# Performance work log

Hardware: AMD Instinct MI355X
Metric: run time of the kernel (lower is better)

## Reference

```python
import jax, jax.numpy as jnp
import numpy as np

NHID = 768
H = 128        # LSTM hidden per direction
NHEADS = 6
NDIR = 12      # 6 heads x 2 directions; first 6 = forward, last 6 = backward
DFF = 4 * NHID
CAT = 2 * H * NHEADS  # 1536


def setup_inputs() -> dict:
    key = jax.random.key(0)
    ks = jax.random.split(key, 12)
    s = 0.05
    return {
        "embeddings": jax.random.normal(ks[0], (16, 512, NHID), jnp.float32),
        # stacked LSTM params; gate order i,f,g,o as in PyTorch
        "W_ih": jax.random.normal(ks[1], (NDIR, 4 * H, NHID), jnp.float32) * s,
        "W_hh": jax.random.normal(ks[2], (NDIR, 4 * H, H), jnp.float32) * s,
        "b_ih": jax.random.normal(ks[3], (NDIR, 4 * H), jnp.float32) * s,
        "b_hh": jax.random.normal(ks[4], (NDIR, 4 * H), jnp.float32) * s,
        "W_int": jax.random.normal(ks[5], (DFF, CAT), jnp.float32) * s,
        "b_int": jax.random.normal(ks[6], (DFF,), jnp.float32) * s,
        "W_out": jax.random.normal(ks[7], (NHID, DFF), jnp.float32) * s,
        "b_out": jax.random.normal(ks[8], (NHID,), jnp.float32) * s,
        "gamma": jnp.ones((NHID,), jnp.float32),
        "beta": jnp.zeros((NHID,), jnp.float32),
    }


def _multi_bilstm(x, W_ih, W_hh, b_ih, b_hh):
    # x: [B,S,D] -> concat of 6 bidirectional LSTM outputs [B,S,1536]
    B, S, _ = x.shape
    # input projections for all 12 directions at once: [12,B,S,4H]
    xp = jnp.einsum('bsd,kgd->kbsg', x, W_ih) + (b_ih + b_hh)[:, None, None, :]
    # reverse time for the 6 backward directions
    xp = jnp.concatenate([xp[:NHEADS], xp[NHEADS:, :, ::-1]], axis=0)
    xs = jnp.moveaxis(xp, 2, 0)  # [S,12,B,4H]

    def step(carry, z_x):
        h, c = carry  # each [12,B,H]
        z = z_x + jnp.einsum('kbh,kgh->kbg', h, W_hh)
        i, f, g, o = jnp.split(z, 4, axis=-1)
        c = jax.nn.sigmoid(f) * c + jax.nn.sigmoid(i) * jnp.tanh(g)
        h = jax.nn.sigmoid(o) * jnp.tanh(c)
        return (h, c), h

    init = (jnp.zeros((NDIR, B, H), x.dtype), jnp.zeros((NDIR, B, H), x.dtype))
    _, ys = jax.lax.scan(step, init, xs)        # [S,12,B,H]
    ys = jnp.moveaxis(ys, 0, 2)                 # [12,B,S,H]
    ys = jnp.concatenate([ys[:NHEADS], ys[NHEADS:, :, ::-1]], axis=0)
    # per-head layout: head0_fwd, head0_bwd, head1_fwd, ... (matches torch.cat of per-LSTM outputs)
    ys = ys.reshape(2, NHEADS, B, S, H).transpose(2, 3, 1, 0, 4)
    return ys.reshape(B, S, CAT)


def reference(embeddings, W_ih, W_hh, b_ih, b_hh, W_int, b_int, W_out, b_out, gamma, beta):
    cat = _multi_bilstm(embeddings, W_ih, W_hh, b_ih, b_hh)
    inter = jax.nn.gelu(cat @ W_int.T + b_int, approximate=False)
    proj = inter @ W_out.T + b_out
    res = embeddings + proj  # dropout is identity (p=0 / eval)
    mu = jnp.mean(res, axis=-1, keepdims=True)
    var = jnp.mean(jnp.square(res - mu), axis=-1, keepdims=True)
    return (res - mu) * jax.lax.rsqrt(var + 1e-5) * gamma + beta
```

## Files before the change

### kernel.cpp

```cpp
#include <hip/hip_runtime.h>

typedef __attribute__((ext_vector_type(4))) float f32x4;
typedef __attribute__((ext_vector_type(8))) short short8;
typedef unsigned short u16;
typedef unsigned int u32;

__device__ __forceinline__ u16 f2bf(float f){
  u32 x = __float_as_uint(f);
  u32 r = x + 0x7fffu + ((x >> 16) & 1u);
  return (u16)(r >> 16);
}
__device__ __forceinline__ float bf2f32(u32 u){ return __uint_as_float(u << 16); }

__device__ __forceinline__ void gld_lds16(const u16* g, u16* l){
  __builtin_amdgcn_global_load_lds((const __attribute__((address_space(1))) void*)g,
                                   (__attribute__((address_space(3))) void*)l, 16, 0, 0);
}

__device__ __forceinline__ f32x4 mfma16(short8 a, short8 b, f32x4 c){
  return __builtin_amdgcn_mfma_f32_16x16x32_bf16(a, b, c, 0, 0, 0);
}

__device__ __forceinline__ float sigf(float x){
  return __builtin_amdgcn_rcpf(1.0f + __expf(-x));
}
__device__ __forceinline__ float tanhf_(float x){
  float e = __expf(2.0f * x);
  return 1.0f - 2.0f * __builtin_amdgcn_rcpf(e + 1.0f);
}

__global__ __launch_bounds__(256) void k_castall(const float* __restrict__ s0, const float* __restrict__ s1,
                          const float* __restrict__ s2, const float* __restrict__ s3,
                          u16* __restrict__ d0, u16* __restrict__ d1, u16* __restrict__ d2,
                          u16* __restrict__ d3)
{
  int i = blockIdx.x * 256 + threadIdx.x;
  const float* s; u16* d; int off;
  if (i < 1572864)      { s = s0; d = d0; off = i; }
  else if (i < 1769472) { s = s1; d = d1; off = i - 1572864; }
  else if (i < 2949120) { s = s2; d = d2; off = i - 1769472; }
  else                  { s = s3; d = d3; off = i - 2949120; }
  float4 v = ((const float4*)s)[off];
  ushort4 o; o.x=f2bf(v.x); o.y=f2bf(v.y); o.z=f2bf(v.z); o.w=f2bf(v.w);
  ((ushort4*)d)[off] = o;
}

__global__ __launch_bounds__(192) void k_permw(const float* __restrict__ wih, u16* __restrict__ dst)
{
  int np = blockIdx.x;
  int d = np >> 9, r = np & 511;
  int src = d*512 + (r & 3)*128 + (r >> 2);
  float4 v = ((const float4*)(wih + (size_t)src*768))[threadIdx.x];
  ushort4 o; o.x=f2bf(v.x); o.y=f2bf(v.y); o.z=f2bf(v.z); o.w=f2bf(v.w);
  ((ushort4*)(dst + (size_t)np*768))[threadIdx.x] = o;
}

template<int TPW>
__global__ __launch_bounds__(512) void k_gemmq(
    const u16* __restrict__ A, const u16* __restrict__ B,
    u16* __restrict__ C,
    const float* __restrict__ bias1, const float* __restrict__ bias2,
    int M, int N, int K, int lda)
{
  __shared__ __align__(16) u16 lA[2][256*64];
  __shared__ __align__(16) u16 lB[2][256*64];
  int nwg = gridDim.x;
  int bid = blockIdx.x;
  int q = nwg >> 3;
  int swz = (bid & 7) * q + (bid >> 3);
  int nbng = N / (256 * TPW);
  int bm = swz / nbng, bng = swz % nbng;
  int tid = threadIdx.x, lane = tid & 63;
  int wv = tid >> 6;
  int wm = wv & 1, wn = wv >> 1;
  int l15 = lane & 15, lhi = lane >> 4;
  const u16* Ag = A + (size_t)(bm << 8) * lda;
  const u16* Bg0 = B + (size_t)(bng * TPW) * 256 * lda;
  size_t bstep = (size_t)256 * lda;

  int srA[4], slA[4];
  #pragma unroll
  for (int i = 0; i < 4; ++i){
    int c = i*512 + tid;
    srA[i] = c >> 3;
    slA[i] = (((c & 7) ^ (srA[i] & 7)) << 3);
  }
  int axr = l15 & 7;
  int aoff0 = (wm*128 + l15)*64 + ((lhi    ) ^ axr)*8;
  int aoff1 = (wm*128 + l15)*64 + ((lhi + 4) ^ axr)*8;
  int boff0 = (wn*64  + l15)*64 + ((lhi    ) ^ axr)*8;
  int boff1 = (wn*64  + l15)*64 + ((lhi + 4) ^ axr)*8;

  f32x4 acc[8][4];
  #pragma unroll
  for (int i = 0; i < 8; ++i)
    #pragma unroll
    for (int j = 0; j < 4; ++j)
      acc[i][j] = (f32x4){0.f,0.f,0.f,0.f};

  int NT = K >> 6;
  int TOT = NT * TPW;

#define STAGE_A(SS)                                                            \
  { int ss_ = (SS); int ko = (ss_ % NT) << 6; u16* dA = lA[ss_ & 1];           \
    _Pragma("unroll")                                                          \
    for (int i = 0; i < 4; ++i)                                                \
      gld_lds16(Ag + (size_t)srA[i]*lda + ko + slA[i], &dA[(i*512+tid)*8]); }
#define STAGE_B(SS)                                                            \
  { int ss_ = (SS); int ko = (ss_ % NT) << 6;                                  \
    const u16* Bb = Bg0 + (size_t)(ss_ / NT) * bstep;                          \
    u16* dB = lB[ss_ & 1];                                                     \
    _Pragma("unroll")                                                          \
    for (int i = 0; i < 4; ++i)                                                \
      gld_lds16(Bb + (size_t)srA[i]*lda + ko + slA[i], &dB[(i*512+tid)*8]); }

  STAGE_A(0)
  STAGE_B(0)
  asm volatile("s_waitcnt vmcnt(0)" ::: "memory");
  __builtin_amdgcn_s_barrier();

  int kt = 0, tile = 0;
  for (int tt = 0; tt < TOT; ++tt){
    const u16* sA = lA[tt & 1];
    const u16* sB = lB[tt & 1];
    short8 bf[4][2];
    #pragma unroll
    for (int p = 0; p < 4; ++p){
      if (p == 0){
        #pragma unroll
        for (int ni = 0; ni < 4; ++ni){
          bf[ni][0] = *(const short8*)&sB[boff0 + ni*1024];
          bf[ni][1] = *(const short8*)&sB[boff1 + ni*1024];
        }
      }
      short8 a00 = *(const short8*)&sA[aoff0 + (2*p)*1024];
      short8 a01 = *(const short8*)&sA[aoff1 + (2*p)*1024];
      short8 a10 = *(const short8*)&sA[aoff0 + (2*p+1)*1024];
      short8 a11 = *(const short8*)&sA[aoff1 + (2*p+1)*1024];
      if (p == 0 && tt + 1 < TOT){ STAGE_A(tt+1) }
      if (p == 1 && tt + 1 < TOT){ STAGE_B(tt+1) }
      __builtin_amdgcn_s_setprio(1);
      #pragma unroll
      for (int ni = 0; ni < 4; ++ni){
        acc[2*p  ][ni] = mfma16(a00, bf[ni][0], acc[2*p  ][ni]);
        acc[2*p  ][ni] = mfma16(a01, bf[ni][1], acc[2*p  ][ni]);
        acc[2*p+1][ni] = mfma16(a10, bf[ni][0], acc[2*p+1][ni]);
        acc[2*p+1][ni] = mfma16(a11, bf[ni][1], acc[2*p+1][ni]);
      }
      __builtin_amdgcn_s_setprio(0);
      if (p == 3 && tt + 1 < TOT){
        asm volatile("s_waitcnt vmcnt(0)" ::: "memory");
      }
      asm volatile("s_barrier" ::: "memory");
    }

    if (kt == NT - 1){
      int bnbase = (bng * TPW + tile) * 256;
      #pragma unroll
      for (int ni = 0; ni < 4; ++ni){
        int n = bnbase + wn*64 + ni*16 + l15;
        int dd = n >> 9, r9 = n & 511;
        int src = dd*512 + (r9 & 3)*128 + (r9 >> 2);
        float bs = bias1[src] + bias2[src];
        #pragma unroll
        for (int mi = 0; mi < 8; ++mi){
          #pragma unroll
          for (int r = 0; r < 4; ++r){
            int m = (bm << 8) + wm*128 + mi*16 + lhi*4 + r;
            C[(size_t)m * N + n] = f2bf(acc[mi][ni][r] + bs);
            acc[mi][ni][r] = 0.f;
          }
        }
      }
      ++tile; kt = 0;
    } else {
      ++kt;
    }
  }
#undef STAGE_A
#undef STAGE_B
}

template<int MODE, int TPW>
__global__ __launch_bounds__(512) void k_gemmp(
    const u16* __restrict__ A, const u16* __restrict__ B,
    void* __restrict__ C, void* __restrict__ C2,
    const float* __restrict__ bias1, const float* __restrict__ bias2,
    int M, int N, int K, int lda)
{
  __shared__ __align__(16) u16 lA[2][256*64];
  __shared__ __align__(16) u16 lB[3][192*64];
  int nwg = gridDim.x;
  int bid = blockIdx.x;
  int half = 0;
  if (MODE == 2){
    int h2 = nwg >> 1;
    half = (bid >= h2) ? 1 : 0;
    bid -= half ? h2 : 0;
    nwg = h2;
  }
  int koff = half * K;
  int q = nwg >> 3;
  int swz = (bid & 7) * q + (bid >> 3);
  int nbng = N / (192 * TPW);
  int bm = swz / nbng, bng = swz % nbng;
  int tid = threadIdx.x, lane = tid & 63;
  int wv = tid >> 6;
  int wm = wv & 1, wn = wv >> 1;
  int l15 = lane & 15, lhi = lane >> 4;
  const u16* Ag = A + (size_t)(bm << 8) * lda + koff;
  const u16* Bg0 = B + (size_t)(bng * TPW) * 192 * lda + koff;
  size_t bstep = (size_t)192 * lda;

  int srA[4], slA[4];
  #pragma unroll
  for (int i = 0; i < 4; ++i){
    int c = i*512 + tid;
    srA[i] = c >> 3;
    slA[i] = (((c & 7) ^ (srA[i] & 7)) << 3);
  }
  int srB[3], slB[3];
  #pragma unroll
  for (int i = 0; i < 3; ++i){
    int c = i*512 + tid;
    srB[i] = c >> 3;
    slB[i] = (((c & 7) ^ (srB[i] & 7)) << 3);
  }
  int axr = l15 & 7;
  int aoff0 = (wm*128 + l15)*64 + ((lhi    ) ^ axr)*8;
  int aoff1 = (wm*128 + l15)*64 + ((lhi + 4) ^ axr)*8;
  int boff0 = (wn*48  + l15)*64 + ((lhi    ) ^ axr)*8;
  int boff1 = (wn*48  + l15)*64 + ((lhi + 4) ^ axr)*8;

  f32x4 acc[8][3];
  #pragma unroll
  for (int i = 0; i < 8; ++i)
    #pragma unroll
    for (int j = 0; j < 3; ++j)
      acc[i][j] = (f32x4){0.f,0.f,0.f,0.f};

  int NT = K >> 6;
  int TOT = NT * TPW;

#define STAGE_A(SS)                                                            \
  { int ss_ = (SS); int ko = (ss_ % NT) << 6; u16* dA = lA[ss_ & 1];           \
    _Pragma("unroll")                                                          \
    for (int i = 0; i < 4; ++i)                                                \
      gld_lds16(Ag + (size_t)srA[i]*lda + ko + slA[i], &dA[(i*512+tid)*8]); }
#define STAGE_B(SS)                                                            \
  { int ss_ = (SS); int ko = (ss_ % NT) << 6;                                  \
    const u16* Bb = Bg0 + (size_t)(ss_ / NT) * bstep;                          \
    u16* dB = lB[ss_ % 3];                                                     \
    _Pragma("unroll")                                                          \
    for (int i = 0; i < 3; ++i)                                                \
      gld_lds16(Bb + (size_t)srB[i]*lda + ko + slB[i], &dB[(i*512+tid)*8]); }

  STAGE_A(0)
  STAGE_B(0)
  STAGE_B(1)
  asm volatile("s_waitcnt vmcnt(3)" ::: "memory");
  __builtin_amdgcn_s_barrier();

  int kt = 0, tile = 0;
  for (int tt = 0; tt < TOT; ++tt){
    const u16* sA = lA[tt & 1];
    const u16* sB = lB[tt % 3];
    short8 bf[3][2];
    #pragma unroll
    for (int p = 0; p < 4; ++p){
      if (p == 0){
        #pragma unroll
        for (int ni = 0; ni < 3; ++ni){
          bf[ni][0] = *(const short8*)&sB[boff0 + ni*1024];
          bf[ni][1] = *(const short8*)&sB[boff1 + ni*1024];
        }
      }
      short8 a00 = *(const short8*)&sA[aoff0 + (2*p)*1024];
      short8 a01 = *(const short8*)&sA[aoff1 + (2*p)*1024];
      short8 a10 = *(const short8*)&sA[aoff0 + (2*p+1)*1024];
      short8 a11 = *(const short8*)&sA[aoff1 + (2*p+1)*1024];
      if (p == 0 && tt + 1 < TOT){ STAGE_A(tt+1) }
      if (p == 1 && tt + 2 < TOT){ STAGE_B(tt+2) }
      __builtin_amdgcn_s_setprio(1);
      #pragma unroll
      for (int ni = 0; ni < 3; ++ni){
        acc[2*p  ][ni] = mfma16(a00, bf[ni][0], acc[2*p  ][ni]);
        acc[2*p  ][ni] = mfma16(a01, bf[ni][1], acc[2*p  ][ni]);
        acc[2*p+1][ni] = mfma16(a10, bf[ni][0], acc[2*p+1][ni]);
        acc[2*p+1][ni] = mfma16(a11, bf[ni][1], acc[2*p+1][ni]);
      }
      __builtin_amdgcn_s_setprio(0);
      if (p == 3){
        if (tt + 2 < TOT){
          asm volatile("s_waitcnt vmcnt(3)" ::: "memory");
        } else if (tt + 1 < TOT){
          asm volatile("s_waitcnt vmcnt(0)" ::: "memory");
        }
      }
      asm volatile("s_barrier" ::: "memory");
    }

    if (kt == NT - 1){
      int bnbase = (bng * TPW + tile) * 192;
      #pragma unroll
      for (int ni = 0; ni < 3; ++ni){
        int n = bnbase + wn*48 + ni*16 + l15;
        float bs = bias1[n];
        #pragma unroll
        for (int mi = 0; mi < 8; ++mi){
          #pragma unroll
          for (int r = 0; r < 4; ++r){
            int m = (bm << 8) + wm*128 + mi*16 + lhi*4 + r;
            float v = acc[mi][ni][r];
            if (MODE == 2){
              if (!half) v += bs;
              ((u16*)(half ? C2 : C))[(size_t)m * N + n] = f2bf(v);
            } else {
              v += bs;
              v = 0.5f * v * (1.0f + erff(v * 0.70710678118f));
              ((u16*)C)[(size_t)m * N + n] = f2bf(v);
            }
            acc[mi][ni][r] = 0.f;
          }
        }
      }
      ++tile; kt = 0;
    } else {
      ++kt;
    }
  }
#undef STAGE_A
#undef STAGE_B
}

__global__ __launch_bounds__(512) void k_scan(const u16* __restrict__ whh, const u16* __restrict__ xp,
                       u16* __restrict__ cat)
{
  __shared__ __align__(16) u16 hb[2][4*144];
  int bid = blockIdx.x;
  int d = bid >> 2, bg = bid & 3;
  int tid = threadIdx.x, lane = tid & 63, w = tid >> 6;
  int l15 = lane & 15, lhi = lane >> 4;

  u16* hbf = (u16*)hb;
  for (int i = tid; i < 2*4*144; i += 512) hbf[i] = 0;

  short8 wf[4][4];
  #pragma unroll
  for (int g = 0; g < 4; ++g)
    #pragma unroll
    for (int kk = 0; kk < 4; ++kk)
      wf[g][kk] = *(const short8*)(whh + ((size_t)d*512 + g*128 + w*16 + l15)*128 + kk*32 + lhi*8);

  int b = bg*4 + lhi;
  int dim = w*16 + l15;
  bool fwd = (d < 6);
  const u16* zbase = xp + (size_t)b*512*6144 + d*512 + dim*4;

  ushort4 Z[4];
  #pragma unroll
  for (int j = 0; j < 4; ++j){
    int s = fwd ? j : 511 - j;
    Z[j] = *(const ushort4*)(zbase + (size_t)s*6144);
  }

  f32x4 a0={0.f,0.f,0.f,0.f}, a1=a0, a2=a0, a3=a0;
  float cr = 0.f;
  int head = fwd ? d : d - 6;
  int posoff = fwd ? 0 : 128;
  size_t catlane = (size_t)b*512*1536 + head*256 + posoff + dim;
  int catoff = fwd ? 0 : 511*1536;
  int catstep = fwd ? 1536 : -1536;

  int hrd = (l15 >> 2)*144 + lhi*8;
  int hwr = lhi*144 + dim;

  __syncthreads();

#define SCAN_STEP(T, RB, WB, S)                                                \
  {                                                                            \
    short8 hf0 = *(const short8*)&hb[RB][hrd + 0*32];                          \
    short8 hf1 = *(const short8*)&hb[RB][hrd + 1*32];                          \
    short8 hf2 = *(const short8*)&hb[RB][hrd + 2*32];                          \
    short8 hf3 = *(const short8*)&hb[RB][hrd + 3*32];                          \
    a0[0] = bf2f32((u32)Z[S].x); a1[0] = bf2f32((u32)Z[S].y);                  \
    a2[0] = bf2f32((u32)Z[S].z); a3[0] = bf2f32((u32)Z[S].w);                  \
    int t4 = (T) + 4; if (t4 > 511) t4 = 511;                                  \
    int s4 = fwd ? t4 : 511 - t4;                                              \
    Z[S] = *(const ushort4*)(zbase + (size_t)s4*6144);                         \
                                  \
    a0 = mfma16(hf0, wf[0][0], a0); a1 = mfma16(hf0, wf[1][0], a1);            \
    a0 = mfma16(hf1, wf[0][1], a0); a1 = mfma16(hf1, wf[1][1], a1);            \
    a0 = mfma16(hf2, wf[0][2], a0); a1 = mfma16(hf2, wf[1][2], a1);            \
    a0 = mfma16(hf3, wf[0][3], a0); a1 = mfma16(hf3, wf[1][3], a1);            \
                  \
    a2 = mfma16(hf0, wf[2][0], a2); a3 = mfma16(hf0, wf[3][0], a3);            \
    float fi = sigf(a0[0]);                                                    \
    a2 = mfma16(hf1, wf[2][1], a2); a3 = mfma16(hf1, wf[3][1], a3);            \
    float ff = sigf(a1[0]);                                                    \
    a2 = mfma16(hf2, wf[2][2], a2); a3 = mfma16(hf2, wf[3][2], a3);            \
    float fc = ff * cr;                                                        \
    a2 = mfma16(hf3, wf[2][3], a2); a3 = mfma16(hf3, wf[3][3], a3);            \
    float tg = tanhf_(a2[0]);                                                  \
    float fo = sigf(a3[0]);                                                    \
    cr = fc + fi*tg;                                                           \
    float hv = fo * tanhf_(cr);                                                \
    u32 hp32;                                                                  \
    asm("v_cvt_pk_bf16_f32 %0, %1, %2" : "=v"(hp32) : "v"(hv), "v"(hv));       \
    u16 hp = (u16)hp32;                                                        \
    hb[WB][hwr] = hp;                                                          \
    cat[catlane + catoff] = hp;                                                \
    catoff += catstep;                                                         \
    asm volatile("s_waitcnt lgkmcnt(0)" ::: "memory");                         \
    __builtin_amdgcn_s_barrier();                                              \
  }

  for (int t = 0; t < 512; t += 4){
    SCAN_STEP(t,   0, 1, 0)
    SCAN_STEP(t+1, 1, 0, 1)
    SCAN_STEP(t+2, 0, 1, 2)
    SCAN_STEP(t+3, 1, 0, 3)
  }
#undef SCAN_STEP
}

__global__ __launch_bounds__(256) void k_ln(const float* __restrict__ emb, const u16* __restrict__ p0,
                     const u16* __restrict__ p1,
                     const float* __restrict__ gamma, const float* __restrict__ beta,
                     float* __restrict__ out)
{
  int row = blockIdx.x, tid = threadIdx.x;
  const float* pe = emb + (size_t)row * 768;
  const u16* pa = p0 + (size_t)row * 768;
  const u16* pb = p1 + (size_t)row * 768;
  float v0 = pe[tid]     + bf2f32(pa[tid])     + bf2f32(pb[tid]);
  float v1 = pe[tid+256] + bf2f32(pa[tid+256]) + bf2f32(pb[tid+256]);
  float v2 = pe[tid+512] + bf2f32(pa[tid+512]) + bf2f32(pb[tid+512]);
  float s = v0+v1+v2, s2 = v0*v0+v1*v1+v2*v2;
  #pragma unroll
  for (int o = 32; o > 0; o >>= 1){ s += __shfl_down(s, o); s2 += __shfl_down(s2, o); }
  __shared__ float rs[4], rq[4];
  int wv = tid >> 6;
  if ((tid & 63) == 0){ rs[wv] = s; rq[wv] = s2; }
  __syncthreads();
  s = rs[0]+rs[1]+rs[2]+rs[3];
  s2 = rq[0]+rq[1]+rq[2]+rq[3];
  float mu = s * (1.0f/768.0f);
  float var = s2 * (1.0f/768.0f) - mu*mu;
  float rr = rsqrtf(var + 1e-5f);
  float* po = out + (size_t)row * 768;
  po[tid]     = (v0-mu)*rr*gamma[tid]     + beta[tid];
  po[tid+256] = (v1-mu)*rr*gamma[tid+256] + beta[tid+256];
  po[tid+512] = (v2-mu)*rr*gamma[tid+512] + beta[tid+512];
}

extern "C" void kernel_launch(void* const* d_in, const int* in_sizes, int n_in,
                              void* d_out, int out_size, void* d_ws, size_t ws_size,
                              hipStream_t stream)
{
  const float* emb   = (const float*)d_in[0];
  const float* W_ih  = (const float*)d_in[1];
  const float* W_hh  = (const float*)d_in[2];
  const float* b_ih  = (const float*)d_in[3];
  const float* b_hh  = (const float*)d_in[4];
  const float* W_int = (const float*)d_in[5];
  const float* b_int = (const float*)d_in[6];
  const float* W_out = (const float*)d_in[7];
  const float* b_out = (const float*)d_in[8];
  const float* gamma = (const float*)d_in[9];
  const float* beta  = (const float*)d_in[10];
  float* out = (float*)d_out;

  char* ws = (char*)d_ws;
  u16* embb  = (u16*)(ws + 0);
  u16* wihb  = (u16*)(ws + 12582912);
  u16* whhb  = (u16*)(ws + 22020096);
  u16* wintb = (u16*)(ws + 23592960);
  u16* woutb = (u16*)(ws + 33030144);
  u16* catb  = (u16*)(ws + 37748736);
  u16* proj1 = (u16*)(ws + 37748736);
  u16* xp    = (u16*)(ws + 62914560);
  u16* interb= (u16*)(ws + 62914560);
  u16* proj0 = (u16*)(ws + 113246208);

  hipLaunchKernelGGL(k_castall, dim3(13824), dim3(256), 0, stream,
                     emb, W_hh, W_int, W_out, embb, whhb, wintb, woutb);
  hipLaunchKernelGGL(k_permw, dim3(6144), dim3(192), 0, stream, W_ih, wihb);

  hipLaunchKernelGGL((k_gemmq<3>), dim3(256), dim3(512), 0, stream,
                     embb, wihb, xp, b_ih, b_hh, 8192, 6144, 768, 768);
  hipLaunchKernelGGL(k_scan, dim3(48), dim3(512), 0, stream, whhb, xp, catb);
  hipLaunchKernelGGL((k_gemmp<1,2>), dim3(256), dim3(512), 0, stream,
                     catb, wintb, (void*)interb, nullptr, b_int, nullptr, 8192, 3072, 1536, 1536);
  hipLaunchKernelGGL((k_gemmp<2,1>), dim3(256), dim3(512), 0, stream,
                     interb, woutb, (void*)proj0, (void*)proj1, b_out, nullptr, 8192, 768, 1536, 3072);
  hipLaunchKernelGGL(k_ln, dim3(8192), dim3(256), 0, stream, emb, proj0, proj1, gamma, beta, out);
}
```

Measured before the change: 495.7 us.

## Overlap W_int/W_out casts with LSTM scan and merge cast kernels

Folds the embedding/W_hh cast and the permuted W_ih cast into one launch. Moves the W_int and W_out bf16 casts into extra blocks of the scan kernel, so they run on CUs the 48 serial scan blocks leave idle. The scan step is also reordered: MFMAs are interleaved across all four gates, all gate nonlinearities are computed after the MFMAs, and the xp prefetch uses a pointer increment with a peeled tail instead of clamped index math. Scan blocks now reserve a large 96 KB shared array they barely use (so the casts in the extra blocks have CU residency), and the casting blocks compete with the latency-bound scan for memory bandwidth.

```diff
diff --git a/kernel.cpp b/kernel.cpp
--- a/kernel.cpp
+++ b/kernel.cpp
@@ -29,30 +29,27 @@
   return 1.0f - 2.0f * __builtin_amdgcn_rcpf(e + 1.0f);
 }
 
-__global__ __launch_bounds__(256) void k_castall(const float* __restrict__ s0, const float* __restrict__ s1,
-                          const float* __restrict__ s2, const float* __restrict__ s3,
-                          u16* __restrict__ d0, u16* __restrict__ d1, u16* __restrict__ d2,
-                          u16* __restrict__ d3)
+__global__ __launch_bounds__(256) void k_cast2(const float* __restrict__ emb, const float* __restrict__ whh,
+                        const float* __restrict__ wih,
+                        u16* __restrict__ embb, u16* __restrict__ whhb, u16* __restrict__ wihb)
 {
-  int i = blockIdx.x * 256 + threadIdx.x;
-  const float* s; u16* d; int off;
-  if (i < 1572864)      { s = s0; d = d0; off = i; }
-  else if (i < 1769472) { s = s1; d = d1; off = i - 1572864; }
-  else if (i < 2949120) { s = s2; d = d2; off = i - 1769472; }
-  else                  { s = s3; d = d3; off = i - 2949120; }
-  float4 v = ((const float4*)s)[off];
-  ushort4 o; o.x=f2bf(v.x); o.y=f2bf(v.y); o.z=f2bf(v.z); o.w=f2bf(v.w);
-  ((ushort4*)d)[off] = o;
-}
-
-__global__ __launch_bounds__(192) void k_permw(const float* __restrict__ wih, u16* __restrict__ dst)
-{
-  int np = blockIdx.x;
-  int d = np >> 9, r = np & 511;
-  int src = d*512 + (r & 3)*128 + (r >> 2);
-  float4 v = ((const float4*)(wih + (size_t)src*768))[threadIdx.x];
-  ushort4 o; o.x=f2bf(v.x); o.y=f2bf(v.y); o.z=f2bf(v.z); o.w=f2bf(v.w);
-  ((ushort4*)(dst + (size_t)np*768))[threadIdx.x] = o;
+  int bid = blockIdx.x, tid = threadIdx.x;
+  if (bid < 6912){
+    int i = bid * 256 + tid;
+    const float* s; u16* d; int off;
+    if (i < 1572864){ s = emb; d = embb; off = i; }
+    else            { s = whh; d = whhb; off = i - 1572864; }
+    float4 v = ((const float4*)s)[off];
+    ushort4 o; o.x=f2bf(v.x); o.y=f2bf(v.y); o.z=f2bf(v.z); o.w=f2bf(v.w);
+    ((ushort4*)d)[off] = o;
+  } else if (tid < 192){
+    int np = bid - 6912;
+    int d = np >> 9, r = np & 511;
+    int src = d*512 + (r & 3)*128 + (r >> 2);
+    float4 v = ((const float4*)(wih + (size_t)src*768))[tid];
+    ushort4 o; o.x=f2bf(v.x); o.y=f2bf(v.y); o.z=f2bf(v.z); o.w=f2bf(v.w);
+    ((ushort4*)(wihb + (size_t)np*768))[tid] = o;
+  }
 }
 
 template<int TPW>
@@ -334,16 +331,32 @@
 }
 
 __global__ __launch_bounds__(512) void k_scan(const u16* __restrict__ whh, const u16* __restrict__ xp,
-                       u16* __restrict__ cat)
+                       u16* __restrict__ cat,
+                       const float* __restrict__ wint, const float* __restrict__ wout,
+                       u16* __restrict__ wintb, u16* __restrict__ woutb)
 {
-  __shared__ __align__(16) u16 hb[2][4*144];
+  __shared__ __align__(16) u16 big[49152];
   int bid = blockIdx.x;
+  int tid = threadIdx.x;
+
+  if (bid >= 48){
+    for (int i = (bid - 48)*512 + tid; i < 1769472; i += 208*512){
+      const float* s; u16* d; int off;
+      if (i < 1179648){ s = wint; d = wintb; off = i; }
+      else            { s = wout; d = woutb; off = i - 1179648; }
+      float4 v = ((const float4*)s)[off];
+      ushort4 o; o.x=f2bf(v.x); o.y=f2bf(v.y); o.z=f2bf(v.z); o.w=f2bf(v.w);
+      ((ushort4*)d)[off] = o;
+    }
+    return;
+  }
+
+  u16* hb = big;
   int d = bid >> 2, bg = bid & 3;
-  int tid = threadIdx.x, lane = tid & 63, w = tid >> 6;
+  int lane = tid & 63, w = tid >> 6;
   int l15 = lane & 15, lhi = lane >> 4;
 
-  u16* hbf = (u16*)hb;
-  for (int i = tid; i < 2*4*144; i += 512) hbf[i] = 0;
+  for (int i = tid; i < 2*576; i += 512) hb[i] = 0;
 
   short8 wf[4][4];
   #pragma unroll
@@ -363,6 +376,8 @@
     int s = fwd ? j : 511 - j;
     Z[j] = *(const ushort4*)(zbase + (size_t)s*6144);
   }
+  const u16* zpre = zbase + (size_t)(fwd ? 4 : 507) * 6144;
+  int zstep = fwd ? 6144 : -6144;
 
   f32x4 a0={0.f,0.f,0.f,0.f}, a1=a0, a2=a0, a3=a0;
   float cr = 0.f;
@@ -377,51 +392,48 @@
 
   __syncthreads();
 
-#define SCAN_STEP(T, RB, WB, S)                                                \
+#define SCAN_BODY(RB, WB, S, PRE)                                              \
   {                                                                            \
-    short8 hf0 = *(const short8*)&hb[RB][hrd + 0*32];                          \
-    short8 hf1 = *(const short8*)&hb[RB][hrd + 1*32];                          \
-    short8 hf2 = *(const short8*)&hb[RB][hrd + 2*32];                          \
-    short8 hf3 = *(const short8*)&hb[RB][hrd + 3*32];                          \
+    short8 hf0 = *(const short8*)&hb[(RB)*576 + hrd + 0*32];                   \
+    short8 hf1 = *(const short8*)&hb[(RB)*576 + hrd + 1*32];                   \
+    short8 hf2 = *(const short8*)&hb[(RB)*576 + hrd + 2*32];                   \
+    short8 hf3 = *(const short8*)&hb[(RB)*576 + hrd + 3*32];                   \
     a0[0] = bf2f32((u32)Z[S].x); a1[0] = bf2f32((u32)Z[S].y);                  \
     a2[0] = bf2f32((u32)Z[S].z); a3[0] = bf2f32((u32)Z[S].w);                  \
-    int t4 = (T) + 4; if (t4 > 511) t4 = 511;                                  \
-    int s4 = fwd ? t4 : 511 - t4;                                              \
-    Z[S] = *(const ushort4*)(zbase + (size_t)s4*6144);                         \
-                                  \
-    a0 = mfma16(hf0, wf[0][0], a0); a1 = mfma16(hf0, wf[1][0], a1);            \
-    a0 = mfma16(hf1, wf[0][1], a0); a1 = mfma16(hf1, wf[1][1], a1);            \
-    a0 = mfma16(hf2, wf[0][2], a0); a1 = mfma16(hf2, wf[1][2], a1);            \
-    a0 = mfma16(hf3, wf[0][3], a0); a1 = mfma16(hf3, wf[1][3], a1);            \
-                  \
-    a2 = mfma16(hf0, wf[2][0], a2); a3 = mfma16(hf0, wf[3][0], a3);            \
-    float fi = sigf(a0[0]);                                                    \
-    a2 = mfma16(hf1, wf[2][1], a2); a3 = mfma16(hf1, wf[3][1], a3);            \
-    float ff = sigf(a1[0]);                                                    \
-    a2 = mfma16(hf2, wf[2][2], a2); a3 = mfma16(hf2, wf[3][2], a3);            \
-    float fc = ff * cr;                                                        \
-    a2 = mfma16(hf3, wf[2][3], a2); a3 = mfma16(hf3, wf[3][3], a3);            \
+    if (PRE){ Z[S] = *(const ushort4*)zpre; zpre += zstep; }                   \
+    a2 = mfma16(hf0, wf[2][0], a2); a0 = mfma16(hf0, wf[0][0], a0);            \
+    a1 = mfma16(hf0, wf[1][0], a1); a3 = mfma16(hf0, wf[3][0], a3);            \
+    a2 = mfma16(hf1, wf[2][1], a2); a0 = mfma16(hf1, wf[0][1], a0);            \
+    a1 = mfma16(hf1, wf[1][1], a1); a3 = mfma16(hf1, wf[3][1], a3);            \
+    a2 = mfma16(hf2, wf[2][2], a2); a0 = mfma16(hf2, wf[0][2], a0);            \
+    a1 = mfma16(hf2, wf[1][2], a1); a3 = mfma16(hf2, wf[3][2], a3);            \
+    a2 = mfma16(hf3, wf[2][3], a2); a0 = mfma16(hf3, wf[0][3], a0);            \
+    a1 = mfma16(hf3, wf[1][3], a1); a3 = mfma16(hf3, wf[3][3], a3);            \
     float tg = tanhf_(a2[0]);                                                  \
-    float fo = sigf(a3[0]);                                                    \
-    cr = fc + fi*tg;                                                           \
+    float fi = sigf(a0[0]), ff = sigf(a1[0]), fo = sigf(a3[0]);                \
+    cr = ff*cr + fi*tg;                                                        \
     float hv = fo * tanhf_(cr);                                                \
     u32 hp32;                                                                  \
     asm("v_cvt_pk_bf16_f32 %0, %1, %2" : "=v"(hp32) : "v"(hv), "v"(hv));       \
     u16 hp = (u16)hp32;                                                        \
-    hb[WB][hwr] = hp;                                                          \
+    hb[(WB)*576 + hwr] = hp;                                                   \
     cat[catlane + catoff] = hp;                                                \
     catoff += catstep;                                                         \
     asm volatile("s_waitcnt lgkmcnt(0)" ::: "memory");                         \
     __builtin_amdgcn_s_barrier();                                              \
   }
 
-  for (int t = 0; t < 512; t += 4){
-    SCAN_STEP(t,   0, 1, 0)
-    SCAN_STEP(t+1, 1, 0, 1)
-    SCAN_STEP(t+2, 0, 1, 2)
-    SCAN_STEP(t+3, 1, 0, 3)
-  }
-#undef SCAN_STEP
+  for (int t = 0; t < 508; t += 4){
+    SCAN_BODY(0, 1, 0, 1)
+    SCAN_BODY(1, 0, 1, 1)
+    SCAN_BODY(0, 1, 2, 1)
+    SCAN_BODY(1, 0, 3, 1)
+  }
+  SCAN_BODY(0, 1, 0, 0)
+  SCAN_BODY(1, 0, 1, 0)
+  SCAN_BODY(0, 1, 2, 0)
+  SCAN_BODY(1, 0, 3, 0)
+#undef SCAN_BODY
 }
 
 __global__ __launch_bounds__(256) void k_ln(const float* __restrict__ emb, const u16* __restrict__ p0,
@@ -483,13 +495,13 @@
   u16* interb= (u16*)(ws + 62914560);
   u16* proj0 = (u16*)(ws + 113246208);
 
-  hipLaunchKernelGGL(k_castall, dim3(13824), dim3(256), 0, stream,
-                     emb, W_hh, W_int, W_out, embb, whhb, wintb, woutb);
-  hipLaunchKernelGGL(k_permw, dim3(6144), dim3(192), 0, stream, W_ih, wihb);
+  hipLaunchKernelGGL(k_cast2, dim3(13056), dim3(256), 0, stream,
+                     emb, W_hh, W_ih, embb, whhb, wihb);
 
   hipLaunchKernelGGL((k_gemmq<3>), dim3(256), dim3(512), 0, stream,
                      embb, wihb, xp, b_ih, b_hh, 8192, 6144, 768, 768);
-  hipLaunchKernelGGL(k_scan, dim3(48), dim3(512), 0, stream, whhb, xp, catb);
+  hipLaunchKernelGGL(k_scan, dim3(256), dim3(512), 0, stream,
+                     whhb, xp, catb, W_int, W_out, wintb, woutb);
   hipLaunchKernelGGL((k_gemmp<1,2>), dim3(256), dim3(512), 0, stream,
                      catb, wintb, (void*)interb, nullptr, b_int, nullptr, 8192, 3072, 1536, 1536);
   hipLaunchKernelGGL((k_gemmp<2,1>), dim3(256), dim3(512), 0, stream,
```

Result: faster. 481.2 us (-2.9%).
